# Kernel tuning notes

Measured on AMD Instinct MI355X. Metric: run time of the kernel, lower is better.

## Reference

```python
import jax, jax.numpy as jnp
import numpy as np

NB = 50  # nb_steps
IN_D = 64
HID = 128
B = 256


def _cc_weights(nb):
    # Faithful port of UMNN compute_cc_weights (Clenshaw-Curtis quadrature)
    lam = np.arange(0, nb + 1).reshape(-1, 1).astype(np.float64)
    lam = np.cos((lam @ lam.T) * np.pi / nb)
    lam[:, 0] = 0.5
    lam[:, -1] = 0.5 * lam[:, -1]
    lam = lam * 2.0 / nb
    W = np.arange(0, nb + 1).reshape(-1, 1).astype(np.float64)
    W[np.arange(1, nb + 1, 2)] = 0
    W = 2.0 / (1.0 - W ** 2)
    W[0] = 1
    W[np.arange(1, nb + 1, 2)] = 0
    cc = (lam.T @ W)[:, 0].astype(np.float32)              # [nb+1]
    steps = np.cos(np.arange(0, nb + 1) * np.pi / nb).astype(np.float32)  # [nb+1]
    return jnp.asarray(cc), jnp.asarray(steps)


def setup_inputs() -> dict:
    key = jax.random.key(0)
    ks = jax.random.split(key, 16)
    d = {}
    d["x"] = jax.random.normal(ks[0], (B, 1), dtype=jnp.float32)
    d["h"] = jax.random.normal(ks[1], (B, IN_D - 1), dtype=jnp.float32)

    def lin(kw, kb, fan_in, fan_out):
        s = 1.0 / np.sqrt(fan_in)
        w = jax.random.uniform(kw, (fan_in, fan_out), jnp.float32, -s, s)
        b = jax.random.uniform(kb, (fan_out,), jnp.float32, -s, s)
        return w, b

    # Integrand MLP: in_d -> 128 -> 128 -> 1
    d["iw0"], d["ib0"] = lin(ks[2], ks[3], IN_D, HID)
    d["iw1"], d["ib1"] = lin(ks[4], ks[5], HID, HID)
    d["iw2"], d["ib2"] = lin(ks[6], ks[7], HID, 1)
    # Outer net: (in_d-1) -> 128 -> 128 -> 2
    d["nw0"], d["nb0"] = lin(ks[8], ks[9], IN_D - 1, HID)
    d["nw1"], d["nb1"] = lin(ks[10], ks[11], HID, HID)
    d["nw2"], d["nb2"] = lin(ks[12], ks[13], HID, 2)
    return d


def reference(x, h, iw0, ib0, iw1, ib1, iw2, ib2, nw0, nb0, nw1, nb1, nw2, nb2):
    cc, steps = _cc_weights(NB)  # [S1], [S1]
    S1 = NB + 1
    b = x.shape[0]

    # ----- outer quadrature: integral over t in [0, x] -----
    # t[b, i] = 0 + (x - 0) * (steps[i] + 1) / 2
    t = x[:, None, :] * (steps[None, :, None] + 1.0) / 2.0          # [B, S1, 1]

    # ----- inner UMNN: integral over s in [t, xmax], xmax = max(t) + 10 -----
    xmax = jnp.max(t) + 10.0
    s = t[:, :, None, :] + (xmax - t)[:, :, None, :] * (steps[None, None, :, None] + 1.0) / 2.0  # [B,S1,S1,1]

    hb = jnp.broadcast_to(h[:, None, None, :], (b, S1, S1, h.shape[1]))
    inp = jnp.concatenate([s, hb], axis=-1)                         # [B,S1,S1,in_d]

    # PostiveIntegrandNN: Lin-ReLU-Lin-ReLU-Lin-ELU, then + 1.0
    a = jax.nn.relu(inp @ iw0 + ib0)
    a = jax.nn.relu(a @ iw1 + ib1)
    f = jax.nn.elu(a @ iw2 + ib2) + 1.0                              # [B,S1,S1,1]

    # inner Clenshaw-Curtis reduction: z * (xT - x0) / 2
    inner = jnp.sum(f * cc[None, None, :, None], axis=2) * (xmax - t) / 2.0   # [B,S1,1]

    # outer reduction: integral from 0 to x
    outer = jnp.sum(inner * cc[None, :, None], axis=1) * x / 2.0    # [B,1]

    # outer dense net on h -> offset / scaling
    o = jax.nn.relu(h @ nw0 + nb0)
    o = jax.nn.relu(o @ nw1 + nb1)
    o = o @ nw2 + nb2                                               # [B,2]
    offset = o[:, 0:1]
    scaling = jnp.exp(o[:, 1:2])
    return scaling * outer + offset
```

## Files before the change

kernel.cpp:

```cpp
#include <hip/hip_runtime.h>
#include <math.h>

#define NBQ 50
#define S1 51
#define NPTS 2601
#define IN_D 64
#define HID 128
#define BSZ 256
#define NCHUNK 8
#define NUMAX 21

typedef __bf16 bf16x8 __attribute__((ext_vector_type(8)));
typedef float  f32x4  __attribute__((ext_vector_type(4)));
typedef unsigned int u32x4 __attribute__((ext_vector_type(4)));

#define WS_CC     0
#define WS_STEPS  64
#define WS_XMAX   128
#define WS_BASE   256
#define WS_SCAL   33024
#define WS_OFF    33280
#define WS_PART   33536
#define WS_W1BF   41728

static __device__ inline unsigned int cvt_pk_bf16(float lo, float hi) {
    unsigned int r;
    asm("v_cvt_pk_bf16_f32 %0, %1, %2" : "=v"(r) : "v"(lo), "v"(hi));
    return r;
}

__global__ void k_prep(const float* __restrict__ x, const float* __restrict__ h,
                       const float* __restrict__ iw0, const float* __restrict__ ib0,
                       const float* __restrict__ iw1,
                       const float* __restrict__ nw0, const float* __restrict__ nb0,
                       const float* __restrict__ nw1, const float* __restrict__ nb1,
                       const float* __restrict__ nw2, const float* __restrict__ nb2,
                       float* __restrict__ ws) {
    int blk = blockIdx.x;
    int tid = threadIdx.x;

    if (blk < 64) {
        int idx  = blk * 256 + tid;
        int e    = idx & 7;
        int lane = (idx >> 3) & 63;
        int fk   = idx >> 9;
        int kk   = fk & 3;
        int nt   = fk >> 2;
        int k = kk * 32 + (lane >> 4) * 8 + e;
        int n = nt * 16 + (lane & 15);
        __bf16* w1bf = (__bf16*)(ws + WS_W1BF);
        w1bf[idx] = (__bf16)iw1[k * HID + n];
        return;
    }

    __shared__ float s_steps[S1];
    __shared__ float s_red[4];
    __shared__ float s_h[IN_D - 1];
    __shared__ float s_o0[HID];
    __shared__ float s_part[4];

    if (blk == 64) {
        int t = tid;
        if (t < S1) {
            double st = cos((double)t * M_PI / (double)NBQ);
            s_steps[t] = (float)st;
            ws[WS_STEPS + t] = (float)st;
            double acc = 0.0;
            for (int i = 0; i <= NBQ; ++i) {
                double Wi;
                if (i == 0)       Wi = 1.0;
                else if (i & 1)   Wi = 0.0;
                else              Wi = 2.0 / (1.0 - (double)i * (double)i);
                double lam;
                if (t == 0)  lam = 0.5;
                else         lam = cos((double)i * (double)t * M_PI / (double)NBQ);
                if (t == NBQ) lam *= 0.5;
                lam *= 2.0 / (double)NBQ;
                acc += lam * Wi;
            }
            ws[WS_CC + t] = (float)acc;
        }
        __syncthreads();
        float xb = x[t];
        float m = -1e30f;
        for (int i = 0; i < S1; ++i)
            m = fmaxf(m, xb * (s_steps[i] + 1.0f) * 0.5f);
        for (int off = 32; off > 0; off >>= 1)
            m = fmaxf(m, __shfl_down(m, off));
        if ((t & 63) == 0) s_red[t >> 6] = m;
        __syncthreads();
        if (t == 0) {
            float mm = fmaxf(fmaxf(s_red[0], s_red[1]), fmaxf(s_red[2], s_red[3]));
            ws[WS_XMAX] = mm + 10.0f;
        }
        return;
    }

    int b = blk - 65;
    int n = tid;
    bool act = (n < HID);
    if (act && n < IN_D - 1) s_h[n] = h[b * (IN_D - 1) + n];
    __syncthreads();
    float o1 = 0.0f;
    if (act) {
        float aB0 = ib0[n], aB1 = 0.f, aB2 = 0.f, aB3 = 0.f;
        float a00 = nb0[n], a01 = 0.f, a02 = 0.f, a03 = 0.f;
        int d = 0;
        for (; d + 4 <= IN_D - 1; d += 4) {
            float h0 = s_h[d], h1 = s_h[d + 1], h2 = s_h[d + 2], h3 = s_h[d + 3];
            aB0 = fmaf(h0, iw0[(1 + d) * HID + n], aB0);
            aB1 = fmaf(h1, iw0[(2 + d) * HID + n], aB1);
            aB2 = fmaf(h2, iw0[(3 + d) * HID + n], aB2);
            aB3 = fmaf(h3, iw0[(4 + d) * HID + n], aB3);
            a00 = fmaf(h0, nw0[(d)     * HID + n], a00);
            a01 = fmaf(h1, nw0[(d + 1) * HID + n], a01);
            a02 = fmaf(h2, nw0[(d + 2) * HID + n], a02);
            a03 = fmaf(h3, nw0[(d + 3) * HID + n], a03);
        }
        for (; d < IN_D - 1; ++d) {
            float hv = s_h[d];
            aB0 = fmaf(hv, iw0[(1 + d) * HID + n], aB0);
            a00 = fmaf(hv, nw0[d * HID + n], a00);
        }
        ws[WS_BASE + b * HID + n] = (aB0 + aB1) + (aB2 + aB3);
        s_o0[n] = fmaxf((a00 + a01) + (a02 + a03), 0.0f);
    }
    __syncthreads();
    if (act) {
        float a0 = nb1[n], a1 = 0.f, a2 = 0.f, a3 = 0.f;
        for (int m = 0; m < HID; m += 4) {
            a0 = fmaf(s_o0[m],     nw1[(m)     * HID + n], a0);
            a1 = fmaf(s_o0[m + 1], nw1[(m + 1) * HID + n], a1);
            a2 = fmaf(s_o0[m + 2], nw1[(m + 2) * HID + n], a2);
            a3 = fmaf(s_o0[m + 3], nw1[(m + 3) * HID + n], a3);
        }
        o1 = fmaxf((a0 + a1) + (a2 + a3), 0.0f);
    }
    float p0 = act ? o1 * nw2[n * 2 + 0] : 0.0f;
    float p1 = act ? o1 * nw2[n * 2 + 1] : 0.0f;
    for (int off = 32; off > 0; off >>= 1) {
        p0 += __shfl_down(p0, off);
        p1 += __shfl_down(p1, off);
    }
    int lane = tid & 63, w = tid >> 6;
    if (lane == 0 && w < 2) { s_part[w * 2] = p0; s_part[w * 2 + 1] = p1; }
    __syncthreads();
    if (tid == 0) {
        ws[WS_OFF + b]  = s_part[0] + s_part[2] + nb2[0];
        ws[WS_SCAL + b] = expf(s_part[1] + s_part[3] + nb2[1]);
    }
}

__global__ __launch_bounds__(256, 4) void k3_mfma(
        const float* __restrict__ x,
        const float* __restrict__ iw0,
        const float* __restrict__ ib1,
        const float* __restrict__ iw2,
        const float* __restrict__ ib2,
        float* __restrict__ ws) {
    __shared__ bf16x8 bfr_lds[4][4][64];
    __shared__ float zlds[4][NUMAX][17];
    __shared__ float s_tbl[NUMAX][16];
    __shared__ float w_tbl[NUMAX][16];
    __shared__ float s_red[4];

    int blk  = blockIdx.x;
    int b    = blk >> 3;
    int c    = blk & 7;
    int tid  = threadIdx.x;
    int wave = tid >> 6;
    int lane = tid & 63;
    int col  = lane & 15;
    int g    = lane >> 4;

    float xmax = ws[WS_XMAX];
    float xb   = x[b];
    float b2   = ib2[0];

    int NU = (c <= 2) ? 21 : 20;
    int G  = (NU + 3) >> 2;

    for (int e = tid; e < NU * 16; e += 256) {
        int u  = e >> 4;
        int cl = e & 15;
        int p  = (c + 8 * u) * 16 + cl;
        int pc = (p < NPTS) ? p : (NPTS - 1);
        int i  = (int)(((unsigned)pc * 10281u) >> 19);
        int j  = pc - i * 51;
        float sti = ws[WS_STEPS + i];
        float stj = ws[WS_STEPS + j];
        float ti  = xb * (sti + 1.0f) * 0.5f;
        float w   = xmax - ti;
        s_tbl[u][cl] = fmaf(w, (stj + 1.0f) * 0.5f, ti);
        w_tbl[u][cl] = (p < NPTS) ? ws[WS_CC + i] * ws[WS_CC + j] * w : 0.0f;
    }

    const bf16x8* w1f = (const bf16x8*)(ws + WS_W1BF);
    bf16x8 Af[2][4];
#pragma unroll
    for (int nt = 0; nt < 2; ++nt) {
        int NT = wave * 2 + nt;
#pragma unroll
        for (int kk = 0; kk < 4; ++kk)
            Af[nt][kk] = w1f[(NT * 4 + kk) * 64 + lane];
    }

    const float* basep = ws + WS_BASE + b * HID;
    int m0 = wave * 32 + g * 8;
    f32x4 w0a = *(const f32x4*)(iw0 + m0);
    f32x4 w0b = *(const f32x4*)(iw0 + m0 + 4);
    f32x4 bsa = *(const f32x4*)(basep + m0);
    f32x4 bsb = *(const f32x4*)(basep + m0 + 4);

    f32x4 accInit[2], iw2v[2];
#pragma unroll
    for (int nt = 0; nt < 2; ++nt) {
        int n0 = (wave * 2 + nt) * 16 + g * 4;
        accInit[nt] = *(const f32x4*)(ib1 + n0);
        iw2v[nt]    = *(const f32x4*)(iw2 + n0);
    }

    __syncthreads();

    for (int grp = 0; grp < G; ++grp) {
        int ubase = grp * 4;
#pragma unroll
        for (int t = 0; t < 4; ++t) {
            int u = ubase + t;
            if (u < NU) {
                float s = s_tbl[u][col];
                float v0 = fmaxf(fmaf(s, w0a[0], bsa[0]), 0.0f);
                float v1 = fmaxf(fmaf(s, w0a[1], bsa[1]), 0.0f);
                float v2 = fmaxf(fmaf(s, w0a[2], bsa[2]), 0.0f);
                float v3 = fmaxf(fmaf(s, w0a[3], bsa[3]), 0.0f);
                float v4 = fmaxf(fmaf(s, w0b[0], bsb[0]), 0.0f);
                float v5 = fmaxf(fmaf(s, w0b[1], bsb[1]), 0.0f);
                float v6 = fmaxf(fmaf(s, w0b[2], bsb[2]), 0.0f);
                float v7 = fmaxf(fmaf(s, w0b[3], bsb[3]), 0.0f);
                u32x4 pk;
                pk[0] = cvt_pk_bf16(v0, v1);
                pk[1] = cvt_pk_bf16(v2, v3);
                pk[2] = cvt_pk_bf16(v4, v5);
                pk[3] = cvt_pk_bf16(v6, v7);
                bfr_lds[t][wave][lane] = __builtin_bit_cast(bf16x8, pk);
            }
        }
        __syncthreads();
#pragma unroll
        for (int t = 0; t < 4; ++t) {
            int u = ubase + t;
            if (u < NU) {
                bf16x8 f0 = bfr_lds[t][0][lane];
                bf16x8 f1 = bfr_lds[t][1][lane];
                bf16x8 f2 = bfr_lds[t][2][lane];
                bf16x8 f3 = bfr_lds[t][3][lane];
                __builtin_amdgcn_s_setprio(1);
                f32x4 a0 = __builtin_amdgcn_mfma_f32_16x16x32_bf16(Af[0][0], f0, accInit[0], 0, 0, 0);
                f32x4 a1 = __builtin_amdgcn_mfma_f32_16x16x32_bf16(Af[1][0], f0, accInit[1], 0, 0, 0);
                a0 = __builtin_amdgcn_mfma_f32_16x16x32_bf16(Af[0][1], f1, a0, 0, 0, 0);
                a1 = __builtin_amdgcn_mfma_f32_16x16x32_bf16(Af[1][1], f1, a1, 0, 0, 0);
                a0 = __builtin_amdgcn_mfma_f32_16x16x32_bf16(Af[0][2], f2, a0, 0, 0, 0);
                a1 = __builtin_amdgcn_mfma_f32_16x16x32_bf16(Af[1][2], f2, a1, 0, 0, 0);
                a0 = __builtin_amdgcn_mfma_f32_16x16x32_bf16(Af[0][3], f3, a0, 0, 0, 0);
                a1 = __builtin_amdgcn_mfma_f32_16x16x32_bf16(Af[1][3], f3, a1, 0, 0, 0);
                __builtin_amdgcn_s_setprio(0);

                float za = 0.f, zb = 0.f;
#pragma unroll
                for (int q = 0; q < 4; ++q) {
                    za = fmaf(fmaxf(a0[q], 0.0f), iw2v[0][q], za);
                    zb = fmaf(fmaxf(a1[q], 0.0f), iw2v[1][q], zb);
                }
                float z = za + zb;
                z += __shfl_xor(z, 16);
                z += __shfl_xor(z, 32);
                if (lane < 16) zlds[wave][u][lane] = z;
            }
        }
        __syncthreads();
    }

    float vsum = 0.0f;
    int npass = (NU + 15) >> 4;
    for (int pass = 0; pass < npass; ++pass) {
        int u = pass * 16 + wave * 4 + g;
        if (u < NU) {
            float z = zlds[0][u][col] + zlds[1][u][col]
                    + zlds[2][u][col] + zlds[3][u][col] + b2;
            float f = (z > 0.0f) ? (z + 1.0f) : __expf(z);
            vsum += w_tbl[u][col] * f;
        }
    }
#pragma unroll
    for (int off = 1; off < 64; off <<= 1)
        vsum += __shfl_xor(vsum, off);
    if (lane == 0) s_red[wave] = vsum;
    __syncthreads();
    if (tid == 0)
        ws[WS_PART + blk] = (s_red[0] + s_red[1] + s_red[2] + s_red[3]) * 0.5f;
}

__global__ void k4_final(const float* __restrict__ x, const float* __restrict__ ws,
                         float* __restrict__ out) {
    int b = threadIdx.x;
    float sum = 0.0f;
#pragma unroll
    for (int c = 0; c < NCHUNK; ++c) sum += ws[WS_PART + b * NCHUNK + c];
    out[b] = ws[WS_SCAL + b] * sum * x[b] * 0.5f + ws[WS_OFF + b];
}

extern "C" void kernel_launch(void* const* d_in, const int* in_sizes, int n_in,
                              void* d_out, int out_size, void* d_ws, size_t ws_size,
                              hipStream_t stream) {
    const float* x   = (const float*)d_in[0];
    const float* h   = (const float*)d_in[1];
    const float* iw0 = (const float*)d_in[2];
    const float* ib0 = (const float*)d_in[3];
    const float* iw1 = (const float*)d_in[4];
    const float* ib1 = (const float*)d_in[5];
    const float* iw2 = (const float*)d_in[6];
    const float* ib2 = (const float*)d_in[7];
    const float* nw0 = (const float*)d_in[8];
    const float* nb0 = (const float*)d_in[9];
    const float* nw1 = (const float*)d_in[10];
    const float* nb1 = (const float*)d_in[11];
    const float* nw2 = (const float*)d_in[12];
    const float* nb2 = (const float*)d_in[13];
    float* ws  = (float*)d_ws;
    float* out = (float*)d_out;

    hipLaunchKernelGGL(k_prep, dim3(64 + 1 + BSZ), dim3(256), 0, stream,
                       x, h, iw0, ib0, iw1, nw0, nb0, nw1, nb1, nw2, nb2, ws);
    hipLaunchKernelGGL(k3_mfma, dim3(BSZ * NCHUNK), dim3(256), 0, stream,
                       x, iw0, ib1, iw2, ib2, ws);
    hipLaunchKernelGGL(k4_final, dim3(1), dim3(BSZ), 0, stream, x, ws, out);
}
```

Before: 50.32 us.

## Drop final reduction kernel via atomics and convert W1 to bf16 in-kernel

Removes the separate k4_final launch by having each k3 block atomically add its scaled partial, with the offset added by chunk 0, into an output zeroed in k_prep. The bf16 repacking of iw1 in k_prep is also removed; each k3 block now loads fp32 iw1 with strided reads and converts to bf16 fragments in registers. This saves one launch and the prep blocks, but adds redundant strided global loads of W1 in all 2048 blocks, makes the summation order nondeterministic through float atomics, and relies on out being zeroed in the previous kernel.

Result: slower. 52.11 us (+3.6%).

```diff
diff --git a/kernel.cpp b/kernel.cpp
--- a/kernel.cpp
+++ b/kernel.cpp
@@ -20,8 +20,6 @@
 #define WS_BASE   256
 #define WS_SCAL   33024
 #define WS_OFF    33280
-#define WS_PART   33536
-#define WS_W1BF   41728
 
 static __device__ inline unsigned int cvt_pk_bf16(float lo, float hi) {
     unsigned int r;
@@ -31,27 +29,12 @@
 
 __global__ void k_prep(const float* __restrict__ x, const float* __restrict__ h,
                        const float* __restrict__ iw0, const float* __restrict__ ib0,
-                       const float* __restrict__ iw1,
                        const float* __restrict__ nw0, const float* __restrict__ nb0,
                        const float* __restrict__ nw1, const float* __restrict__ nb1,
                        const float* __restrict__ nw2, const float* __restrict__ nb2,
-                       float* __restrict__ ws) {
+                       float* __restrict__ ws, float* __restrict__ out) {
     int blk = blockIdx.x;
     int tid = threadIdx.x;
-
-    if (blk < 64) {
-        int idx  = blk * 256 + tid;
-        int e    = idx & 7;
-        int lane = (idx >> 3) & 63;
-        int fk   = idx >> 9;
-        int kk   = fk & 3;
-        int nt   = fk >> 2;
-        int k = kk * 32 + (lane >> 4) * 8 + e;
-        int n = nt * 16 + (lane & 15);
-        __bf16* w1bf = (__bf16*)(ws + WS_W1BF);
-        w1bf[idx] = (__bf16)iw1[k * HID + n];
-        return;
-    }
 
     __shared__ float s_steps[S1];
     __shared__ float s_red[4];
@@ -59,8 +42,9 @@
     __shared__ float s_o0[HID];
     __shared__ float s_part[4];
 
-    if (blk == 64) {
+    if (blk == 0) {
         int t = tid;
+        out[t] = 0.0f;
         if (t < S1) {
             double st = cos((double)t * M_PI / (double)NBQ);
             s_steps[t] = (float)st;
@@ -81,22 +65,22 @@
             ws[WS_CC + t] = (float)acc;
         }
         __syncthreads();
-        float xb = x[t];
+        float xb = x[tid];
         float m = -1e30f;
         for (int i = 0; i < S1; ++i)
             m = fmaxf(m, xb * (s_steps[i] + 1.0f) * 0.5f);
         for (int off = 32; off > 0; off >>= 1)
             m = fmaxf(m, __shfl_down(m, off));
-        if ((t & 63) == 0) s_red[t >> 6] = m;
+        if ((tid & 63) == 0) s_red[tid >> 6] = m;
         __syncthreads();
-        if (t == 0) {
+        if (tid == 0) {
             float mm = fmaxf(fmaxf(s_red[0], s_red[1]), fmaxf(s_red[2], s_red[3]));
             ws[WS_XMAX] = mm + 10.0f;
         }
         return;
     }
 
-    int b = blk - 65;
+    int b = blk - 1;
     int n = tid;
     bool act = (n < HID);
     if (act && n < IN_D - 1) s_h[n] = h[b * (IN_D - 1) + n];
@@ -154,10 +138,12 @@
 __global__ __launch_bounds__(256, 4) void k3_mfma(
         const float* __restrict__ x,
         const float* __restrict__ iw0,
+        const float* __restrict__ iw1,
         const float* __restrict__ ib1,
         const float* __restrict__ iw2,
         const float* __restrict__ ib2,
-        float* __restrict__ ws) {
+        float* __restrict__ ws,
+        float* __restrict__ out) {
     __shared__ bf16x8 bfr_lds[4][4][64];
     __shared__ float zlds[4][NUMAX][17];
     __shared__ float s_tbl[NUMAX][16];
@@ -195,14 +181,23 @@
         w_tbl[u][cl] = (p < NPTS) ? ws[WS_CC + i] * ws[WS_CC + j] * w : 0.0f;
     }
 
-    const bf16x8* w1f = (const bf16x8*)(ws + WS_W1BF);
     bf16x8 Af[2][4];
 #pragma unroll
     for (int nt = 0; nt < 2; ++nt) {
-        int NT = wave * 2 + nt;
-#pragma unroll
-        for (int kk = 0; kk < 4; ++kk)
-            Af[nt][kk] = w1f[(NT * 4 + kk) * 64 + lane];
+        int n = (wave * 2 + nt) * 16 + col;
+        const float* src = iw1 + n + (g * 8) * HID;
+#pragma unroll
+        for (int kk = 0; kk < 4; ++kk) {
+            const float* sk = src + (kk * 32) * HID;
+            u32x4 pk;
+#pragma unroll
+            for (int e2 = 0; e2 < 4; ++e2) {
+                float lo = sk[(2 * e2) * HID];
+                float hi = sk[(2 * e2 + 1) * HID];
+                pk[e2] = cvt_pk_bf16(lo, hi);
+            }
+            Af[nt][kk] = __builtin_bit_cast(bf16x8, pk);
+        }
     }
 
     const float* basep = ws + WS_BASE + b * HID;
@@ -296,17 +291,13 @@
         vsum += __shfl_xor(vsum, off);
     if (lane == 0) s_red[wave] = vsum;
     __syncthreads();
-    if (tid == 0)
-        ws[WS_PART + blk] = (s_red[0] + s_red[1] + s_red[2] + s_red[3]) * 0.5f;
-}
-
-__global__ void k4_final(const float* __restrict__ x, const float* __restrict__ ws,
-                         float* __restrict__ out) {
-    int b = threadIdx.x;
-    float sum = 0.0f;
-#pragma unroll
-    for (int c = 0; c < NCHUNK; ++c) sum += ws[WS_PART + b * NCHUNK + c];
-    out[b] = ws[WS_SCAL + b] * sum * x[b] * 0.5f + ws[WS_OFF + b];
+
+    if (tid == 0) {
+        float part = (s_red[0] + s_red[1] + s_red[2] + s_red[3]) * 0.25f;
+        float contrib = ws[WS_SCAL + b] * part * xb;
+        if (c == 0) contrib += ws[WS_OFF + b];
+        atomicAdd(&out[b], contrib);
+    }
 }
 
 extern "C" void kernel_launch(void* const* d_in, const int* in_sizes, int n_in,
@@ -329,9 +320,8 @@
     float* ws  = (float*)d_ws;
     float* out = (float*)d_out;
 
-    hipLaunchKernelGGL(k_prep, dim3(64 + 1 + BSZ), dim3(256), 0, stream,
-                       x, h, iw0, ib0, iw1, nw0, nb0, nw1, nb1, nw2, nb2, ws);
+    hipLaunchKernelGGL(k_prep, dim3(1 + BSZ), dim3(256), 0, stream,
+                       x, h, iw0, ib0, nw0, nb0, nw1, nb1, nw2, nb2, ws, out);
     hipLaunchKernelGGL(k3_mfma, dim3(BSZ * NCHUNK), dim3(256), 0, stream,
-                       x, iw0, ib1, iw2, ib2, ws);
-    hipLaunchKernelGGL(k4_final, dim3(1), dim3(BSZ), 0, stream, x, ws, out);
+                       x, iw0, iw1, ib1, iw2, ib2, ws, out);
 }
```
